# Kernel optimization log

Hardware: AMD Instinct MI355X
Metric: run time of the kernel (lower is better)

Reference implementation:

```python
import jax, jax.numpy as jnp
import numpy as np

N, E, G = 50000, 400000, 500
F_IN, D_H, D_EMB = 92, 256, 128
EPS = 1e-5

def _ln(x, g, b):
    # per-node LayerNorm over feature dim
    mu = jnp.mean(x, axis=-1, keepdims=True)
    var = jnp.mean(jnp.square(x - mu), axis=-1, keepdims=True)
    return (x - mu) * jax.lax.rsqrt(var + EPS) * g + b

def _gcn_conv(x, src, dst, W, b):
    # PyG GCNConv: add self-loops, symmetric normalization
    xw = x @ W                                    # [N, D_out]
    loop = jnp.arange(N, dtype=src.dtype)
    s = jnp.concatenate([src, loop])              # [E+N]
    d = jnp.concatenate([dst, loop])
    deg = jax.ops.segment_sum(jnp.ones_like(d, dtype=xw.dtype), d, num_segments=N)
    dinv = jnp.where(deg > 0, jax.lax.rsqrt(jnp.maximum(deg, 1.0)) * (deg > 0), 0.0)
    norm = dinv[s] * dinv[d]                      # [E+N]
    msg = xw[s] * norm[:, None]                   # gather + scale
    out = jax.ops.segment_sum(msg, d, num_segments=N)  # scatter-add
    return out + b

def setup_inputs() -> dict:
    key = jax.random.key(0)
    ks = jax.random.split(key, 12)
    def lin(k, fan_in, fan_out):
        bound = 1.0 / np.sqrt(fan_in)
        kw, kb = jax.random.split(k)
        W = jax.random.uniform(kw, (fan_in, fan_out), jnp.float32, -bound, bound)
        b = jax.random.uniform(kb, (fan_out,), jnp.float32, -bound, bound)
        return W, b
    x = jax.random.normal(ks[0], (N, F_IN), jnp.float32)
    edge_index = jax.random.randint(ks[1], (2, E), 0, N, jnp.int32)
    batch = jnp.sort(jax.random.randint(ks[2], (N,), 0, G, jnp.int32))
    nfc_W, nfc_b = lin(ks[3], F_IN, D_H)
    gc1_W, gc1_b = lin(ks[4], D_H, D_H)
    gc2_W, gc2_b = lin(ks[5], D_H, D_EMB)
    fc1_W, fc1_b = lin(ks[6], D_EMB, 64)
    fc2_W, fc2_b = lin(ks[7], 64, 1)
    return {
        "x": x, "edge_index": edge_index, "batch": batch,
        "nfc_W": nfc_W, "nfc_b": nfc_b,
        "gn1_g": jnp.ones((D_H,), jnp.float32), "gn1_b": jnp.zeros((D_H,), jnp.float32),
        "gc1_W": gc1_W, "gc1_b": gc1_b,
        "gn2_g": jnp.ones((D_EMB,), jnp.float32), "gn2_b": jnp.zeros((D_EMB,), jnp.float32),
        "gc2_W": gc2_W, "gc2_b": gc2_b,
        "fc1_W": fc1_W, "fc1_b": fc1_b,
        "fc2_W": fc2_W, "fc2_b": fc2_b,
    }

def reference(x, edge_index, batch, nfc_W, nfc_b, gn1_g, gn1_b, gc1_W, gc1_b,
              gn2_g, gn2_b, gc2_W, gc2_b, fc1_W, fc1_b, fc2_W, fc2_b):
    src, dst = edge_index[0], edge_index[1]
    lrelu = jax.nn.leaky_relu  # slope 0.01, matches F.leaky_relu default
    ha = lrelu(x @ nfc_W + nfc_b)
    ha = lrelu(_ln(_gcn_conv(ha, src, dst, gc1_W, gc1_b), gn1_g, gn1_b))
    ha = lrelu(_ln(_gcn_conv(ha, src, dst, gc2_W, gc2_b), gn2_g, gn2_b))
    # F.normalize(p=2, dim=1)
    ha = ha / jnp.maximum(jnp.linalg.norm(ha, axis=1, keepdims=True), 1e-12)
    hg = jax.ops.segment_sum(ha, batch, num_segments=G)   # global_add_pool
    h = lrelu(hg @ fc1_W + fc1_b)
    out = h @ fc2_W + fc2_b
    return out, ha
```

## Files before the change

kernel.cpp:

```cpp
#include <hip/hip_runtime.h>

#define NN 50000
#define EE 400000
#define GG 500
#define F_IN 92
#define KP1 96
#define D_H 256
#define D_EMB 128

typedef __attribute__((ext_vector_type(8))) short short8_t;
typedef __attribute__((ext_vector_type(4))) float floatx4;
typedef unsigned short u16;
typedef unsigned int u32;

__device__ __forceinline__ float lrelu(float v) { return v > 0.f ? v : 0.01f * v; }
__device__ __forceinline__ u16 f2b(float v) {
    union { float f; u32 u; } x; x.f = v;
    u32 r = x.u + 0x7FFFu + ((x.u >> 16) & 1u);
    return (u16)(r >> 16);
}
__device__ __forceinline__ float wave_allsum(float v) {
#pragma unroll
    for (int m = 1; m < 64; m <<= 1) v += __shfl_xor(v, m);
    return v;
}
__device__ __forceinline__ void glds16(const void* g, void* l) {
    __builtin_amdgcn_global_load_lds(
        (const __attribute__((address_space(1))) void*)g,
        (__attribute__((address_space(3))) void*)l, 16, 0, 0);
}

__global__ void scan1(const int* __restrict__ cnt, int* __restrict__ excl,
                      int* __restrict__ bsum, float* __restrict__ dinv, int n) {
    __shared__ int sm[256];
    int i = blockIdx.x * 256 + threadIdx.x;
    int v = (i < n) ? cnt[i] : 0;
    if (i < n) dinv[i] = rsqrtf((float)v + 1.0f);
    sm[threadIdx.x] = v;
    __syncthreads();
#pragma unroll
    for (int off = 1; off < 256; off <<= 1) {
        int t = (threadIdx.x >= off) ? sm[threadIdx.x - off] : 0;
        __syncthreads();
        sm[threadIdx.x] += t;
        __syncthreads();
    }
    if (i < n) excl[i] = sm[threadIdx.x] - v;
    if (threadIdx.x == 255) bsum[blockIdx.x] = sm[255];
}
__global__ void scan2(int* __restrict__ bsum, int nb) {
    __shared__ int sm[256];
    int v = (threadIdx.x < nb) ? bsum[threadIdx.x] : 0;
    sm[threadIdx.x] = v;
    __syncthreads();
#pragma unroll
    for (int off = 1; off < 256; off <<= 1) {
        int t = (threadIdx.x >= off) ? sm[threadIdx.x - off] : 0;
        __syncthreads();
        sm[threadIdx.x] += t;
        __syncthreads();
    }
    if (threadIdx.x < nb) bsum[threadIdx.x] = sm[threadIdx.x] - v;
}
__global__ void scan3(int* __restrict__ rowptr, const int* __restrict__ bsum, int n, int E) {
    int i = blockIdx.x * 256 + threadIdx.x;
    if (i < n) rowptr[i] += bsum[blockIdx.x];
    if (i == 0) rowptr[n] = E;
}

#define WN_ELEMS (D_H * KP1)
#define W1_ELEMS (D_H * D_H)
#define W2_ELEMS (D_EMB * D_H)
__global__ void cast_all(const float* __restrict__ nfc_W, const float* __restrict__ gc1_W,
                         const float* __restrict__ gc2_W, u16* __restrict__ WtN,
                         u16* __restrict__ Wt1, u16* __restrict__ Wt2) {
    int i = blockIdx.x * blockDim.x + threadIdx.x;
    if (i < WN_ELEMS) {
        int n = i / KP1, k = i % KP1;
        WtN[i] = f2b(k < F_IN ? nfc_W[(long)k * D_H + n] : 0.f);
    } else if (i < WN_ELEMS + W1_ELEMS) {
        int j = i - WN_ELEMS;
        int n = j / D_H, k = j % D_H;
        Wt1[j] = f2b(gc1_W[(long)k * D_H + n]);
    } else if (i < WN_ELEMS + W1_ELEMS + W2_ELEMS) {
        int j = i - WN_ELEMS - W1_ELEMS;
        int n = j / D_H, k = j % D_H;
        Wt2[j] = f2b(gc2_W[(long)k * D_EMB + n]);
    }
}

__global__ __launch_bounds__(256) void gemm_f32a(const float* __restrict__ Af_,
                                                 const u16* __restrict__ Wt,
                                                 const float* __restrict__ bias,
                                                 u16* __restrict__ out,
                                                 const int* __restrict__ dstE,
                                                 int* __restrict__ cnt,
                                                 int MBLK) {
    if ((int)blockIdx.x >= MBLK) {
        int e = (blockIdx.x - MBLK) * 256 + threadIdx.x;
        if (e < EE) atomicAdd(&cnt[dstE[e]], 1);
        return;
    }
    __shared__ u16 As[128][40];
    __shared__ u16 Bs[256][32];
    int tid = threadIdx.x;
    int wave = tid >> 6, lane = tid & 63;
    int lm = lane & 15, lk = lane >> 4;
    int m0 = blockIdx.x * 128;
    int rowA = tid >> 1, skA = (tid & 1) * 16;
    int lr = lane >> 2, lc = (lane & 3) * 8;
    int gmA = m0 + rowA;
    const float* Af = Af_ + (size_t)gmA * F_IN;
    const u16* Bp[4];
#pragma unroll
    for (int ch = 0; ch < 4; ++ch)
        Bp[ch] = Wt + (size_t)(wave * 64 + ch * 16 + lr) * KP1 + lc;
    floatx4 acc[2][16] = {};
    for (int k0 = 0; k0 < KP1; k0 += 32) {
        float f[16];
#pragma unroll
        for (int q = 0; q < 4; ++q) {
            int col = k0 + skA + 4 * q;
            float4 t = make_float4(0.f, 0.f, 0.f, 0.f);
            if (gmA < NN && col < F_IN) t = *(const float4*)(Af + col);
            f[4 * q] = t.x; f[4 * q + 1] = t.y; f[4 * q + 2] = t.z; f[4 * q + 3] = t.w;
        }
        u32 pk[8];
#pragma unroll
        for (int t2 = 0; t2 < 8; ++t2)
            pk[t2] = ((u32)f2b(f[2 * t2 + 1]) << 16) | f2b(f[2 * t2]);
        __syncthreads();
        *(uint4*)&As[rowA][skA] = make_uint4(pk[0], pk[1], pk[2], pk[3]);
        *(uint4*)&As[rowA][skA + 8] = make_uint4(pk[4], pk[5], pk[6], pk[7]);
#pragma unroll
        for (int ch = 0; ch < 4; ++ch)
            glds16(Bp[ch] + k0, &Bs[wave * 64 + ch * 16][0]);
        __syncthreads();
        short8_t af0 = *(const short8_t*)&As[wave * 32 + lm][lk * 8];
        short8_t af1 = *(const short8_t*)&As[wave * 32 + 16 + lm][lk * 8];
#pragma unroll
        for (int c = 0; c < 16; ++c) {
            short8_t bf = *(const short8_t*)&Bs[c * 16 + lm][lk * 8];
            acc[0][c] = __builtin_amdgcn_mfma_f32_16x16x32_bf16(af0, bf, acc[0][c], 0, 0, 0);
            acc[1][c] = __builtin_amdgcn_mfma_f32_16x16x32_bf16(af1, bf, acc[1][c], 0, 0, 0);
        }
    }
#pragma unroll
    for (int h = 0; h < 2; ++h) {
#pragma unroll
        for (int r = 0; r < 4; ++r) {
            int gm = m0 + wave * 32 + h * 16 + lk * 4 + r;
            if (gm >= NN) continue;
#pragma unroll
            for (int c = 0; c < 16; ++c) {
                int gn = c * 16 + lm;
                float v = acc[h][c][r] + bias[gn];
                out[(size_t)gm * D_H + gn] = f2b(lrelu(v));
            }
        }
    }
}

template <int ND, bool SCAT>
__global__ __launch_bounds__(256) void gemm_glds(const u16* __restrict__ A,
                                                 const u16* __restrict__ Wt,
                                                 const float* __restrict__ rscale,
                                                 u16* __restrict__ out,
                                                 const int* __restrict__ srcE,
                                                 const int* __restrict__ dstE,
                                                 const int* __restrict__ rowptr,
                                                 int* __restrict__ cursor,
                                                 int* __restrict__ esrc,
                                                 int MBLK) {
    if constexpr (SCAT) {
        if ((int)blockIdx.x >= MBLK) {
            int e = (blockIdx.x - MBLK) * 256 + threadIdx.x;
            if (e < EE) {
                int d = dstE[e];
                int p = rowptr[d] + atomicAdd(&cursor[d], 1);
                esrc[p] = srcE[e];
            }
            return;
        }
    }
    constexpr int NC  = ND / 16;
    constexpr int BCH = ND / 64;
    __shared__ u16 As[2][128][32];
    __shared__ u16 Bs[2][ND][32];
    int tid = threadIdx.x;
    int wave = tid >> 6, lane = tid & 63;
    int lm = lane & 15, lk = lane >> 4;
    int m0 = blockIdx.x * 128;
    int lr = lane >> 2;
    int lc = (lane & 3) * 8;
    const int Ka = D_H;
    const u16* ApA = A + (size_t)(m0 + wave * 32 + lr) * Ka + lc;
    const u16* ApB = A + (size_t)(m0 + wave * 32 + 16 + lr) * Ka + lc;
    const u16* Bp[BCH];
#pragma unroll
    for (int ch = 0; ch < BCH; ++ch)
        Bp[ch] = Wt + (size_t)(wave * (ND / 4) + ch * 16 + lr) * Ka + lc;

    auto stage = [&](int b, int k0) {
        glds16(ApA + k0, &As[b][wave * 32][0]);
        glds16(ApB + k0, &As[b][wave * 32 + 16][0]);
#pragma unroll
        for (int ch = 0; ch < BCH; ++ch)
            glds16(Bp[ch] + k0, &Bs[b][wave * (ND / 4) + ch * 16][0]);
    };

    floatx4 acc[2][NC] = {};
    constexpr int nk = D_H / 32;
    stage(0, 0);
    asm volatile("s_waitcnt vmcnt(0)" ::: "memory");
    __builtin_amdgcn_s_barrier();
    __builtin_amdgcn_sched_barrier(0);
    int cur = 0;
    for (int t = 0; t < nk; ++t) {
        if (t + 1 < nk) stage(cur ^ 1, (t + 1) * 32);
        short8_t af0 = *(const short8_t*)&As[cur][wave * 32 + lm][lk * 8];
        short8_t af1 = *(const short8_t*)&As[cur][wave * 32 + 16 + lm][lk * 8];
#pragma unroll
        for (int c = 0; c < NC; ++c) {
            short8_t bf = *(const short8_t*)&Bs[cur][c * 16 + lm][lk * 8];
            acc[0][c] = __builtin_amdgcn_mfma_f32_16x16x32_bf16(af0, bf, acc[0][c], 0, 0, 0);
            acc[1][c] = __builtin_amdgcn_mfma_f32_16x16x32_bf16(af1, bf, acc[1][c], 0, 0, 0);
        }
        if (t + 1 < nk) {
            __builtin_amdgcn_sched_barrier(0);
            asm volatile("s_waitcnt vmcnt(0)" ::: "memory");
            __builtin_amdgcn_s_barrier();
            __builtin_amdgcn_sched_barrier(0);
            cur ^= 1;
        }
    }
#pragma unroll
    for (int h = 0; h < 2; ++h) {
#pragma unroll
        for (int r = 0; r < 4; ++r) {
            int gm = m0 + wave * 32 + h * 16 + lk * 4 + r;
            if (gm >= NN) continue;
            float rs = rscale[gm];
#pragma unroll
            for (int c = 0; c < NC; ++c) {
                int gn = c * 16 + lm;
                out[(size_t)gm * ND + gn] = f2b(acc[h][c][r] * rs);
            }
        }
    }
}

template <int U>
__device__ __forceinline__ void loadrow(const u32* __restrict__ p, u32* r) {
    if constexpr (U == 2) { uint2 t = *(const uint2*)p; r[0] = t.x; r[1] = t.y; }
    else                  { r[0] = *p; }
}
template <int D, bool L2N, bool TOBF, bool POOL>
__global__ __launch_bounds__(256) void agg_ln(const u16* __restrict__ y,
                                              const int* __restrict__ rowptr,
                                              const int* __restrict__ esrc,
                                              const float* __restrict__ dinv,
                                              const float* __restrict__ bias,
                                              const float* __restrict__ gamma,
                                              const float* __restrict__ beta,
                                              u16* __restrict__ outb,
                                              float* __restrict__ outf,
                                              const int* __restrict__ batch,
                                              float* __restrict__ hg) {
    constexpr int V = D / 64;
    constexpr int U = V / 2;
    constexpr int RW = D / 2;
    int wave = threadIdx.x >> 6, lane = threadIdx.x & 63;
    int i = blockIdx.x * 4 + wave;
    if constexpr (!POOL) { if (i >= NN) return; }
    int beg = __builtin_amdgcn_readfirstlane(rowptr[i]);
    int end = __builtin_amdgcn_readfirstlane(rowptr[i + 1]);
    const u32* yu = (const u32*)y;
    const int lu = lane * U;
    float accL[U] = {}, accH[U] = {};
    u32 r[8][U];
    int k = beg;
    for (; k + 7 < end; k += 8) {
#pragma unroll
        for (int q = 0; q < 8; ++q) loadrow<U>(yu + (size_t)esrc[k + q] * RW + lu, r[q]);
#pragma unroll
        for (int j = 0; j < U; ++j) {
            float sL = 0.f, sH = 0.f;
#pragma unroll
            for (int q = 0; q < 8; ++q) {
                sL += __uint_as_float(r[q][j] << 16);
                sH += __uint_as_float(r[q][j] & 0xFFFF0000u);
            }
            accL[j] += sL; accH[j] += sH;
        }
    }
    for (; k + 3 < end; k += 4) {
#pragma unroll
        for (int q = 0; q < 4; ++q) loadrow<U>(yu + (size_t)esrc[k + q] * RW + lu, r[q]);
#pragma unroll
        for (int j = 0; j < U; ++j) {
            accL[j] += (__uint_as_float(r[0][j] << 16) + __uint_as_float(r[1][j] << 16))
                     + (__uint_as_float(r[2][j] << 16) + __uint_as_float(r[3][j] << 16));
            accH[j] += (__uint_as_float(r[0][j] & 0xFFFF0000u) + __uint_as_float(r[1][j] & 0xFFFF0000u))
                     + (__uint_as_float(r[2][j] & 0xFFFF0000u) + __uint_as_float(r[3][j] & 0xFFFF0000u));
        }
    }
    for (; k < end; ++k) {
        loadrow<U>(yu + (size_t)esrc[k] * RW + lu, r[0]);
#pragma unroll
        for (int j = 0; j < U; ++j) {
            accL[j] += __uint_as_float(r[0][j] << 16);
            accH[j] += __uint_as_float(r[0][j] & 0xFFFF0000u);
        }
    }
    loadrow<U>(yu + (size_t)i * RW + lu, r[0]);
#pragma unroll
    for (int j = 0; j < U; ++j) {
        accL[j] += __uint_as_float(r[0][j] << 16);
        accH[j] += __uint_as_float(r[0][j] & 0xFFFF0000u);
    }
    float di = dinv[i];
    float xv[V], lsum = 0.f;
#pragma unroll
    for (int j = 0; j < U; ++j) {
        xv[2 * j]     = accL[j] * di + bias[lane * V + 2 * j];
        xv[2 * j + 1] = accH[j] * di + bias[lane * V + 2 * j + 1];
    }
#pragma unroll
    for (int v = 0; v < V; ++v) lsum += xv[v];
    float mu = wave_allsum(lsum) * (1.0f / D);
    float l2 = 0.f;
#pragma unroll
    for (int v = 0; v < V; ++v) { xv[v] -= mu; l2 += xv[v] * xv[v]; }
    float rstd = rsqrtf(wave_allsum(l2) * (1.0f / D) + 1e-5f);
    float yv[V], ss = 0.f;
#pragma unroll
    for (int v = 0; v < V; ++v) {
        float t = xv[v] * rstd * gamma[lane * V + v] + beta[lane * V + v];
        t = lrelu(t);
        yv[v] = t; ss += t * t;
    }
    if constexpr (L2N) {
        float inv = 1.0f / fmaxf(sqrtf(wave_allsum(ss)), 1e-12f);
#pragma unroll
        for (int v = 0; v < V; ++v) yv[v] *= inv;
    }
    if constexpr (TOBF) {
        if constexpr (V == 4) {
            *(ushort4*)(outb + (size_t)i * D + lane * V) =
                make_ushort4(f2b(yv[0]), f2b(yv[1]), f2b(yv[2]), f2b(yv[3]));
        } else {
            *(ushort2*)(outb + (size_t)i * D + lane * V) = make_ushort2(f2b(yv[0]), f2b(yv[1]));
        }
    } else {
        if constexpr (V == 2) {
            *(float2*)(outf + (size_t)i * D + lane * V) = make_float2(yv[0], yv[1]);
        } else {
            *(float4*)(outf + (size_t)i * D + lane * V) = make_float4(yv[0], yv[1], yv[2], yv[3]);
        }
    }
    if constexpr (POOL) {
        __shared__ float psm[4][D_EMB];
        __shared__ int pb[4];
        psm[wave][lane * 2]     = yv[0];
        psm[wave][lane * 2 + 1] = yv[1];
        if (lane == 0) pb[wave] = batch[i];
        __syncthreads();
        int tid = threadIdx.x;
        if (tid < D_EMB) {
            float acc = psm[0][tid];
            int cur = pb[0];
#pragma unroll
            for (int w = 1; w < 4; ++w) {
                if (pb[w] != cur) {
                    atomicAdd(&hg[(size_t)cur * D_EMB + tid], acc);
                    acc = 0.f; cur = pb[w];
                }
                acc += psm[w][tid];
            }
            atomicAdd(&hg[(size_t)cur * D_EMB + tid], acc);
        }
    }
}

__global__ __launch_bounds__(64) void head_kernel(const float* __restrict__ hg,
                                                  const float* __restrict__ fc1W,
                                                  const float* __restrict__ fc1b,
                                                  const float* __restrict__ fc2W,
                                                  const float* __restrict__ fc2b,
                                                  float* __restrict__ out) {
    int g = blockIdx.x;
    int j = threadIdx.x;
    float h = fc1b[j];
#pragma unroll 8
    for (int k = 0; k < D_EMB; ++k) h += hg[(size_t)g * D_EMB + k] * fc1W[k * 64 + j];
    h = lrelu(h) * fc2W[j];
#pragma unroll
    for (int m = 1; m < 64; m <<= 1) h += __shfl_xor(h, m);
    if (j == 0) out[g] = h + fc2b[0];
}

static inline size_t align256(size_t x) { return (x + 255) & ~(size_t)255; }

extern "C" void kernel_launch(void* const* d_in, const int* in_sizes, int n_in,
                              void* d_out, int out_size, void* d_ws, size_t ws_size,
                              hipStream_t stream) {
    const float* x     = (const float*)d_in[0];
    const int*   ei    = (const int*)d_in[1];
    const int*   batch = (const int*)d_in[2];
    const float* nfc_W = (const float*)d_in[3];
    const float* nfc_b = (const float*)d_in[4];
    const float* gn1_g = (const float*)d_in[5];
    const float* gn1_b = (const float*)d_in[6];
    const float* gc1_W = (const float*)d_in[7];
    const float* gc1_b = (const float*)d_in[8];
    const float* gn2_g = (const float*)d_in[9];
    const float* gn2_b = (const float*)d_in[10];
    const float* gc2_W = (const float*)d_in[11];
    const float* gc2_b = (const float*)d_in[12];
    const float* fc1_W = (const float*)d_in[13];
    const float* fc1_b = (const float*)d_in[14];
    const float* fc2_W = (const float*)d_in[15];
    const float* fc2_b = (const float*)d_in[16];

    char* ws = (char*)d_ws;
    size_t off = 0;
    int*   cnt    = (int*)(ws + off);   off += (size_t)NN * 4;
    int*   cursor = (int*)(ws + off);   off += (size_t)NN * 4;
    float* hg     = (float*)(ws + off); off += align256((size_t)GG * D_EMB * 4);
    float* dinv   = (float*)(ws + off); off += align256((size_t)NN * 4);
    int*   rowptr = (int*)(ws + off);   off += align256((size_t)(NN + 1) * 4);
    int*   bsum   = (int*)(ws + off);   off += align256((size_t)256 * 4);
    int*   esrc   = (int*)(ws + off);   off += align256((size_t)EE * 4);
    u16*   WtN    = (u16*)(ws + off);   off += align256((size_t)D_H * KP1 * 2);
    u16*   Wt1    = (u16*)(ws + off);   off += align256((size_t)D_H * D_H * 2);
    u16*   Wt2    = (u16*)(ws + off);   off += align256((size_t)D_EMB * D_H * 2);
    u16*   ha1b   = (u16*)(ws + off);   off += align256((size_t)NN * D_H * 2);
    u16*   y1b    = (u16*)(ws + off);   off += align256((size_t)NN * D_H * 2);
    u16*   ha2b   = (u16*)(ws + off);   off += align256((size_t)NN * D_H * 2);
    u16*   y2b    = (u16*)(ws + off);   off += align256((size_t)NN * D_EMB * 2);

    const int* src = ei;
    const int* dst = ei + EE;
    float* out_scores = (float*)d_out;
    float* out_ha     = (float*)d_out + GG;

    const int NB = (NN + 255) / 256;
    const int MB = (NN + 127) / 128;
    const int EB = (EE + 255) / 256;
    const size_t zbytes = (size_t)NN * 8 + (size_t)GG * D_EMB * 4;

    hipMemsetAsync(cnt, 0, zbytes, stream);
    cast_all<<<(WN_ELEMS + W1_ELEMS + W2_ELEMS + 255) / 256, 256, 0, stream>>>(
        nfc_W, gc1_W, gc2_W, WtN, Wt1, Wt2);

    gemm_f32a<<<MB + EB, 256, 0, stream>>>(x, WtN, nfc_b, ha1b, dst, cnt, MB);

    scan1<<<NB, 256, 0, stream>>>(cnt, rowptr, bsum, dinv, NN);
    scan2<<<1, 256, 0, stream>>>(bsum, NB);
    scan3<<<NB, 256, 0, stream>>>(rowptr, bsum, NN, EE);

    gemm_glds<D_H, true><<<MB + EB, 256, 0, stream>>>(
        ha1b, Wt1, dinv, y1b, src, dst, rowptr, cursor, esrc, MB);
    agg_ln<D_H, false, true, false><<<NN / 4, 256, 0, stream>>>(
        y1b, rowptr, esrc, dinv, gc1_b, gn1_g, gn1_b, ha2b, nullptr, nullptr, nullptr);

    gemm_glds<D_EMB, false><<<MB, 256, 0, stream>>>(
        ha2b, Wt2, dinv, y2b, nullptr, nullptr, nullptr, nullptr, nullptr, MB);
    agg_ln<D_EMB, true, false, true><<<NN / 4, 256, 0, stream>>>(
        y2b, rowptr, esrc, dinv, gc2_b, gn2_g, gn2_b, nullptr, out_ha, batch, hg);

    head_kernel<<<GG, 64, 0, stream>>>(hg, fc1_W, fc1_b, fc2_W, fc2_b, out_scores);
}
```

Before: 253.2 us.

## Fuse degree count into weight cast, scan into first GEMM, halve GEMM M-tile

The edge degree-count atomics move into the weight-cast kernel, and the per-block scan plus dinv computation run as extra blocks of the first GEMM launch. The second and third scan passes become a single kernel in which each block reduces the preceding block sums itself. Together these cut the launch count from six small kernels to three. All GEMMs also drop from a 128-row to a 64-row tile per block, which doubles the grid for more parallelism but lowers operand reuse per block.

New measurement: 259.2 us. 2.4% more time.

```diff
diff --git a/kernel.cpp b/kernel.cpp
--- a/kernel.cpp
+++ b/kernel.cpp
@@ -7,6 +7,7 @@
 #define KP1 96
 #define D_H 256
 #define D_EMB 128
+#define NB_SCAN 196
 
 typedef __attribute__((ext_vector_type(8))) short short8_t;
 typedef __attribute__((ext_vector_type(4))) float floatx4;
@@ -30,50 +31,19 @@
         (__attribute__((address_space(3))) void*)l, 16, 0, 0);
 }
 
-__global__ void scan1(const int* __restrict__ cnt, int* __restrict__ excl,
-                      int* __restrict__ bsum, float* __restrict__ dinv, int n) {
-    __shared__ int sm[256];
-    int i = blockIdx.x * 256 + threadIdx.x;
-    int v = (i < n) ? cnt[i] : 0;
-    if (i < n) dinv[i] = rsqrtf((float)v + 1.0f);
-    sm[threadIdx.x] = v;
-    __syncthreads();
-#pragma unroll
-    for (int off = 1; off < 256; off <<= 1) {
-        int t = (threadIdx.x >= off) ? sm[threadIdx.x - off] : 0;
-        __syncthreads();
-        sm[threadIdx.x] += t;
-        __syncthreads();
-    }
-    if (i < n) excl[i] = sm[threadIdx.x] - v;
-    if (threadIdx.x == 255) bsum[blockIdx.x] = sm[255];
-}
-__global__ void scan2(int* __restrict__ bsum, int nb) {
-    __shared__ int sm[256];
-    int v = (threadIdx.x < nb) ? bsum[threadIdx.x] : 0;
-    sm[threadIdx.x] = v;
-    __syncthreads();
-#pragma unroll
-    for (int off = 1; off < 256; off <<= 1) {
-        int t = (threadIdx.x >= off) ? sm[threadIdx.x - off] : 0;
-        __syncthreads();
-        sm[threadIdx.x] += t;
-        __syncthreads();
-    }
-    if (threadIdx.x < nb) bsum[threadIdx.x] = sm[threadIdx.x] - v;
-}
-__global__ void scan3(int* __restrict__ rowptr, const int* __restrict__ bsum, int n, int E) {
-    int i = blockIdx.x * 256 + threadIdx.x;
-    if (i < n) rowptr[i] += bsum[blockIdx.x];
-    if (i == 0) rowptr[n] = E;
-}
-
 #define WN_ELEMS (D_H * KP1)
 #define W1_ELEMS (D_H * D_H)
 #define W2_ELEMS (D_EMB * D_H)
-__global__ void cast_all(const float* __restrict__ nfc_W, const float* __restrict__ gc1_W,
-                         const float* __restrict__ gc2_W, u16* __restrict__ WtN,
-                         u16* __restrict__ Wt1, u16* __restrict__ Wt2) {
+#define CAST_BLK ((WN_ELEMS + W1_ELEMS + W2_ELEMS + 255) / 256)
+__global__ void cast_count(const float* __restrict__ nfc_W, const float* __restrict__ gc1_W,
+                           const float* __restrict__ gc2_W, u16* __restrict__ WtN,
+                           u16* __restrict__ Wt1, u16* __restrict__ Wt2,
+                           const int* __restrict__ dstE, int* __restrict__ cnt) {
+    if ((int)blockIdx.x >= CAST_BLK) {
+        int e = (blockIdx.x - CAST_BLK) * 256 + threadIdx.x;
+        if (e < EE) atomicAdd(&cnt[dstE[e]], 1);
+        return;
+    }
     int i = blockIdx.x * blockDim.x + threadIdx.x;
     if (i < WN_ELEMS) {
         int n = i / KP1, k = i % KP1;
@@ -93,21 +63,37 @@
                                                  const u16* __restrict__ Wt,
                                                  const float* __restrict__ bias,
                                                  u16* __restrict__ out,
-                                                 const int* __restrict__ dstE,
-                                                 int* __restrict__ cnt,
+                                                 const int* __restrict__ cnt,
+                                                 int* __restrict__ rowptr,
+                                                 int* __restrict__ bsum,
+                                                 float* __restrict__ dinv,
                                                  int MBLK) {
     if ((int)blockIdx.x >= MBLK) {
-        int e = (blockIdx.x - MBLK) * 256 + threadIdx.x;
-        if (e < EE) atomicAdd(&cnt[dstE[e]], 1);
+        __shared__ int sm[256];
+        int b = blockIdx.x - MBLK;
+        int i = b * 256 + threadIdx.x;
+        int v = (i < NN) ? cnt[i] : 0;
+        if (i < NN) dinv[i] = rsqrtf((float)v + 1.0f);
+        sm[threadIdx.x] = v;
+        __syncthreads();
+#pragma unroll
+        for (int off = 1; off < 256; off <<= 1) {
+            int t = (threadIdx.x >= off) ? sm[threadIdx.x - off] : 0;
+            __syncthreads();
+            sm[threadIdx.x] += t;
+            __syncthreads();
+        }
+        if (i < NN) rowptr[i] = sm[threadIdx.x] - v;
+        if (threadIdx.x == 255) bsum[b] = sm[255];
         return;
     }
-    __shared__ u16 As[128][40];
+    __shared__ u16 As[64][40];
     __shared__ u16 Bs[256][32];
     int tid = threadIdx.x;
     int wave = tid >> 6, lane = tid & 63;
     int lm = lane & 15, lk = lane >> 4;
-    int m0 = blockIdx.x * 128;
-    int rowA = tid >> 1, skA = (tid & 1) * 16;
+    int m0 = blockIdx.x * 64;
+    int rowA = tid >> 2, skA = (tid & 3) * 8;
     int lr = lane >> 2, lc = (lane & 3) * 8;
     int gmA = m0 + rowA;
     const float* Af = Af_ + (size_t)gmA * F_IN;
@@ -115,50 +101,61 @@
 #pragma unroll
     for (int ch = 0; ch < 4; ++ch)
         Bp[ch] = Wt + (size_t)(wave * 64 + ch * 16 + lr) * KP1 + lc;
-    floatx4 acc[2][16] = {};
+    floatx4 acc[16] = {};
     for (int k0 = 0; k0 < KP1; k0 += 32) {
-        float f[16];
-#pragma unroll
-        for (int q = 0; q < 4; ++q) {
+        float f[8];
+#pragma unroll
+        for (int q = 0; q < 2; ++q) {
             int col = k0 + skA + 4 * q;
             float4 t = make_float4(0.f, 0.f, 0.f, 0.f);
             if (gmA < NN && col < F_IN) t = *(const float4*)(Af + col);
             f[4 * q] = t.x; f[4 * q + 1] = t.y; f[4 * q + 2] = t.z; f[4 * q + 3] = t.w;
         }
-        u32 pk[8];
-#pragma unroll
-        for (int t2 = 0; t2 < 8; ++t2)
+        u32 pk[4];
+#pragma unroll
+        for (int t2 = 0; t2 < 4; ++t2)
             pk[t2] = ((u32)f2b(f[2 * t2 + 1]) << 16) | f2b(f[2 * t2]);
         __syncthreads();
         *(uint4*)&As[rowA][skA] = make_uint4(pk[0], pk[1], pk[2], pk[3]);
-        *(uint4*)&As[rowA][skA + 8] = make_uint4(pk[4], pk[5], pk[6], pk[7]);
 #pragma unroll
         for (int ch = 0; ch < 4; ++ch)
             glds16(Bp[ch] + k0, &Bs[wave * 64 + ch * 16][0]);
         __syncthreads();
-        short8_t af0 = *(const short8_t*)&As[wave * 32 + lm][lk * 8];
-        short8_t af1 = *(const short8_t*)&As[wave * 32 + 16 + lm][lk * 8];
+        short8_t af = *(const short8_t*)&As[wave * 16 + lm][lk * 8];
 #pragma unroll
         for (int c = 0; c < 16; ++c) {
             short8_t bf = *(const short8_t*)&Bs[c * 16 + lm][lk * 8];
-            acc[0][c] = __builtin_amdgcn_mfma_f32_16x16x32_bf16(af0, bf, acc[0][c], 0, 0, 0);
-            acc[1][c] = __builtin_amdgcn_mfma_f32_16x16x32_bf16(af1, bf, acc[1][c], 0, 0, 0);
-        }
-    }
-#pragma unroll
-    for (int h = 0; h < 2; ++h) {
-#pragma unroll
-        for (int r = 0; r < 4; ++r) {
-            int gm = m0 + wave * 32 + h * 16 + lk * 4 + r;
-            if (gm >= NN) continue;
-#pragma unroll
-            for (int c = 0; c < 16; ++c) {
-                int gn = c * 16 + lm;
-                float v = acc[h][c][r] + bias[gn];
-                out[(size_t)gm * D_H + gn] = f2b(lrelu(v));
-            }
-        }
-    }
+            acc[c] = __builtin_amdgcn_mfma_f32_16x16x32_bf16(af, bf, acc[c], 0, 0, 0);
+        }
+    }
+#pragma unroll
+    for (int r = 0; r < 4; ++r) {
+        int gm = m0 + wave * 16 + lk * 4 + r;
+        if (gm >= NN) continue;
+#pragma unroll
+        for (int c = 0; c < 16; ++c) {
+            int gn = c * 16 + lm;
+            float v = acc[c][r] + bias[gn];
+            out[(size_t)gm * D_H + gn] = f2b(lrelu(v));
+        }
+    }
+}
+
+__global__ void scan23(int* __restrict__ rowptr, const int* __restrict__ bsum) {
+    __shared__ int sm[256];
+    int b = blockIdx.x;
+    int v = ((int)threadIdx.x < b) ? bsum[threadIdx.x] : 0;
+    sm[threadIdx.x] = v;
+    __syncthreads();
+#pragma unroll
+    for (int off = 128; off > 0; off >>= 1) {
+        if ((int)threadIdx.x < off) sm[threadIdx.x] += sm[threadIdx.x + off];
+        __syncthreads();
+    }
+    int base = sm[0];
+    int i = b * 256 + threadIdx.x;
+    if (i < NN) rowptr[i] += base;
+    if (i == 0) rowptr[NN] = EE;
 }
 
 template <int ND, bool SCAT>
@@ -185,31 +182,29 @@
     }
     constexpr int NC  = ND / 16;
     constexpr int BCH = ND / 64;
-    __shared__ u16 As[2][128][32];
+    __shared__ u16 As[2][64][32];
     __shared__ u16 Bs[2][ND][32];
     int tid = threadIdx.x;
     int wave = tid >> 6, lane = tid & 63;
     int lm = lane & 15, lk = lane >> 4;
-    int m0 = blockIdx.x * 128;
+    int m0 = blockIdx.x * 64;
     int lr = lane >> 2;
     int lc = (lane & 3) * 8;
     const int Ka = D_H;
-    const u16* ApA = A + (size_t)(m0 + wave * 32 + lr) * Ka + lc;
-    const u16* ApB = A + (size_t)(m0 + wave * 32 + 16 + lr) * Ka + lc;
+    const u16* Ap = A + (size_t)(m0 + wave * 16 + lr) * Ka + lc;
     const u16* Bp[BCH];
 #pragma unroll
     for (int ch = 0; ch < BCH; ++ch)
         Bp[ch] = Wt + (size_t)(wave * (ND / 4) + ch * 16 + lr) * Ka + lc;
 
     auto stage = [&](int b, int k0) {
-        glds16(ApA + k0, &As[b][wave * 32][0]);
-        glds16(ApB + k0, &As[b][wave * 32 + 16][0]);
+        glds16(Ap + k0, &As[b][wave * 16][0]);
 #pragma unroll
         for (int ch = 0; ch < BCH; ++ch)
             glds16(Bp[ch] + k0, &Bs[b][wave * (ND / 4) + ch * 16][0]);
     };
 
-    floatx4 acc[2][NC] = {};
+    floatx4 acc[NC] = {};
     constexpr int nk = D_H / 32;
     stage(0, 0);
     asm volatile("s_waitcnt vmcnt(0)" ::: "memory");
@@ -218,13 +213,11 @@
     int cur = 0;
     for (int t = 0; t < nk; ++t) {
         if (t + 1 < nk) stage(cur ^ 1, (t + 1) * 32);
-        short8_t af0 = *(const short8_t*)&As[cur][wave * 32 + lm][lk * 8];
-        short8_t af1 = *(const short8_t*)&As[cur][wave * 32 + 16 + lm][lk * 8];
+        short8_t af = *(const short8_t*)&As[cur][wave * 16 + lm][lk * 8];
 #pragma unroll
         for (int c = 0; c < NC; ++c) {
             short8_t bf = *(const short8_t*)&Bs[cur][c * 16 + lm][lk * 8];
-            acc[0][c] = __builtin_amdgcn_mfma_f32_16x16x32_bf16(af0, bf, acc[0][c], 0, 0, 0);
-            acc[1][c] = __builtin_amdgcn_mfma_f32_16x16x32_bf16(af1, bf, acc[1][c], 0, 0, 0);
+            acc[c] = __builtin_amdgcn_mfma_f32_16x16x32_bf16(af, bf, acc[c], 0, 0, 0);
         }
         if (t + 1 < nk) {
             __builtin_amdgcn_sched_barrier(0);
@@ -235,17 +228,14 @@
         }
     }
 #pragma unroll
-    for (int h = 0; h < 2; ++h) {
-#pragma unroll
-        for (int r = 0; r < 4; ++r) {
-            int gm = m0 + wave * 32 + h * 16 + lk * 4 + r;
-            if (gm >= NN) continue;
-            float rs = rscale[gm];
-#pragma unroll
-            for (int c = 0; c < NC; ++c) {
-                int gn = c * 16 + lm;
-                out[(size_t)gm * ND + gn] = f2b(acc[h][c][r] * rs);
-            }
+    for (int r = 0; r < 4; ++r) {
+        int gm = m0 + wave * 16 + lk * 4 + r;
+        if (gm >= NN) continue;
+        float rs = rscale[gm];
+#pragma unroll
+        for (int c = 0; c < NC; ++c) {
+            int gn = c * 16 + lm;
+            out[(size_t)gm * ND + gn] = f2b(acc[c][r] * rs);
         }
     }
 }
@@ -445,20 +435,18 @@
     float* out_scores = (float*)d_out;
     float* out_ha     = (float*)d_out + GG;
 
-    const int NB = (NN + 255) / 256;
-    const int MB = (NN + 127) / 128;
+    const int MB = (NN + 63) / 64;
     const int EB = (EE + 255) / 256;
     const size_t zbytes = (size_t)NN * 8 + (size_t)GG * D_EMB * 4;
 
     hipMemsetAsync(cnt, 0, zbytes, stream);
-    cast_all<<<(WN_ELEMS + W1_ELEMS + W2_ELEMS + 255) / 256, 256, 0, stream>>>(
-        nfc_W, gc1_W, gc2_W, WtN, Wt1, Wt2);
-
-    gemm_f32a<<<MB + EB, 256, 0, stream>>>(x, WtN, nfc_b, ha1b, dst, cnt, MB);
-
-    scan1<<<NB, 256, 0, stream>>>(cnt, rowptr, bsum, dinv, NN);
-    scan2<<<1, 256, 0, stream>>>(bsum, NB);
-    scan3<<<NB, 256, 0, stream>>>(rowptr, bsum, NN, EE);
+    cast_count<<<CAST_BLK + EB, 256, 0, stream>>>(
+        nfc_W, gc1_W, gc2_W, WtN, Wt1, Wt2, dst, cnt);
+
+    gemm_f32a<<<MB + NB_SCAN, 256, 0, stream>>>(
+        x, WtN, nfc_b, ha1b, cnt, rowptr, bsum, dinv, MB);
+
+    scan23<<<NB_SCAN, 256, 0, stream>>>(rowptr, bsum);
 
     gemm_glds<D_H, true><<<MB + EB, 256, 0, stream>>>(
         ha1b, Wt1, dinv, y1b, src, dst, rowptr, cursor, esrc, MB);
```
